# Kernel optimization log

Measured on AMD Instinct MI355X. Metric: run time of the kernel, lower is better.

## Reference

```python
import jax, jax.numpy as jnp
import numpy as np

B, T, E = 4, 2048, 2048
H, HKV, HD = 16, 8, 128
THETA = 10000.0
SCALE_BASE = 512.0


def _rotate_half(x):
    x1, x2 = jnp.split(x, 2, axis=-1)
    return jnp.concatenate([-x2, x1], axis=-1)


def _xpos_tables(seqlen):
    # cos/sin/scale tables for XPos rotary, all [seqlen, HD], fp32 compute dtype
    half_idx = jnp.arange(0, HD, 2, dtype=jnp.float32)
    inv_freq = 1.0 / (THETA ** (half_idx / HD))            # [HD/2]
    t = jnp.arange(seqlen, dtype=jnp.float32)
    freqs = jnp.outer(t, inv_freq)                          # [seqlen, HD/2]
    emb = jnp.concatenate([freqs, freqs], axis=-1)          # [seqlen, HD]
    cos, sin = jnp.cos(emb), jnp.sin(emb)
    # xpos decay: ((2i + 0.4d)/(1.4d)) ** ((t - L/2)/scale_base)
    scale_vec = (half_idx + 0.4 * HD) / (1.4 * HD)          # [HD/2]
    power = (t - seqlen // 2) / SCALE_BASE                  # [seqlen]
    scale = scale_vec[None, :] ** power[:, None]            # [seqlen, HD/2]
    scale = jnp.concatenate([scale, scale], axis=-1)        # [seqlen, HD]
    return cos, sin, scale


def setup_inputs() -> dict:
    key = jax.random.key(0)
    ks = jax.random.split(key, 5)
    std = 0.02
    return {
        "x": jax.random.normal(ks[0], (B, T, E), dtype=jnp.float32),
        "W_q": jax.random.normal(ks[1], (E, H * HD), dtype=jnp.float32) * std,
        "W_k": jax.random.normal(ks[2], (E, HKV * HD), dtype=jnp.float32) * std,
        "W_v": jax.random.normal(ks[3], (E, HKV * HD), dtype=jnp.float32) * std,
        "W_o": jax.random.normal(ks[4], (E, E), dtype=jnp.float32) * std,
    }


def reference(x, W_q, W_k, W_v, W_o):
    b, t, _ = x.shape
    q = (x @ W_q).reshape(b, t, H, HD)       # [B,T,H,HD]
    k = (x @ W_k).reshape(b, t, HKV, HD)     # [B,T,HKV,HD]
    v = (x @ W_v).reshape(b, t, HKV, HD)
    rep = H // HKV                            # GQA: repeat_interleave over head dim
    k = jnp.repeat(k, rep, axis=2)
    v = jnp.repeat(v, rep, axis=2)

    cos, sin, scale = _xpos_tables(t)         # past_len = 0 (no kv cache)
    cos = cos[None, :, None, :]
    sin = sin[None, :, None, :]
    scale = scale[None, :, None, :]
    q = q * scale
    q = q * cos + _rotate_half(q) * sin
    k = k / scale
    k = k * cos + _rotate_half(k) * sin

    inv_sqrt_d = 1.0 / jnp.sqrt(jnp.float32(HD))
    scores = jnp.einsum('bqhd,bkhd->bhqk', q, k) * inv_sqrt_d  # [B,H,T,T]
    causal = jnp.triu(jnp.ones((t, t), dtype=bool), k=1)
    scores = jnp.where(causal[None, None], -jnp.inf, scores)
    probs = jax.nn.softmax(scores, axis=-1)
    attn = jnp.einsum('bhqk,bkhd->bqhd', probs, v)             # [B,T,H,HD]
    out = attn.reshape(b, t, E) @ W_o
    return out
```

## Files before the change

### kernel.cpp

```cpp
#include <hip/hip_runtime.h>

typedef _Float16 f16;
typedef __attribute__((ext_vector_type(8))) _Float16 f16x8;
typedef __attribute__((ext_vector_type(4))) _Float16 f16x4;
typedef __attribute__((ext_vector_type(4))) float f32x4;
typedef __attribute__((ext_vector_type(16))) float f32x16;
typedef __attribute__((ext_vector_type(4))) unsigned u32x4;

#define T_SEQ 2048
#define NBATCH 4

__device__ __forceinline__ void gld_lds16(const f16* g, f16* l) {
    __builtin_amdgcn_global_load_lds((const __attribute__((address_space(1))) void*)g,
                                     (__attribute__((address_space(3))) void*)l, 16, 0, 0);
}

__device__ __forceinline__ unsigned pk2(float a, float b) {
    __attribute__((ext_vector_type(2))) __fp16 h = __builtin_amdgcn_cvt_pkrtz(a, b);
    return __builtin_bit_cast(unsigned, h);
}

__global__ __launch_bounds__(256) void k_prep(const float* __restrict__ x,
                                              const float* __restrict__ Wq,
                                              const float* __restrict__ Wk,
                                              const float* __restrict__ Wv,
                                              const float* __restrict__ Wo,
                                              f16* __restrict__ xh,
                                              f16* __restrict__ wqkvT,
                                              f16* __restrict__ woT,
                                              float* __restrict__ tab) {
    __shared__ float tile[32][33];
    int bidx = blockIdx.x;
    if (bidx < 16384) {
        int i = bidx * 256 + threadIdx.x;
        float4 v = ((const float4*)x)[i];
        f16x4 o = { (f16)v.x, (f16)v.y, (f16)v.z, (f16)v.w };
        ((f16x4*)xh)[i] = o;
        return;
    }
    bidx -= 16384;
    if (bidx >= 12288) {
        int i = (bidx - 12288) * 256 + threadIdx.x;
        int t = i >> 6, f = i & 63;
        float inv_freq = powf(10000.0f, -(2.0f * f) / 128.0f);
        float ang = (float)t * inv_freq;
        float sv = (2.0f * f + 51.2f) / 179.2f;
        float pw = ((float)t - 1024.0f) / 512.0f;
        tab[i] = cosf(ang);
        tab[131072 + i] = sinf(ang);
        tab[262144 + i] = powf(sv, pw);
        return;
    }
    const float* src; f16* dst; int N, bx, by;
    if (bidx < 4096)      { src = Wq; dst = wqkvT;                      N = 2048; bx = bidx & 63; by = bidx >> 6; }
    else if (bidx < 6144) { src = Wk; dst = wqkvT + (size_t)2048 * 2048; N = 1024; int t2 = bidx - 4096; bx = t2 & 31; by = t2 >> 5; }
    else if (bidx < 8192) { src = Wv; dst = wqkvT + (size_t)3072 * 2048; N = 1024; int t2 = bidx - 6144; bx = t2 & 31; by = t2 >> 5; }
    else                  { src = Wo; dst = woT;                        N = 2048; int t2 = bidx - 8192; bx = t2 & 63; by = t2 >> 6; }
    int n0 = bx * 32, k0 = by * 32;
    int tx = threadIdx.x & 31, ty = threadIdx.x >> 5;
#pragma unroll
    for (int j = 0; j < 32; j += 8)
        tile[ty + j][tx] = src[(size_t)(k0 + ty + j) * N + n0 + tx];
    __syncthreads();
#pragma unroll
    for (int j = 0; j < 32; j += 8)
        dst[(size_t)(n0 + ty + j) * 2048 + k0 + tx] = (f16)tile[tx][ty + j];
}

__global__ __launch_bounds__(256) void k_post(f16* __restrict__ qkv,
                                              f16* __restrict__ vtg,
                                              const float* __restrict__ tab) {
    int bidx = blockIdx.x;
    const int tid = threadIdx.x;
    if (bidx < 1024) {
        const int kt = bidx & 31, bk = bidx >> 5;
        const int b = bk >> 3, kvh = bk & 7;
        __shared__ f16 tile[64][132];
#pragma unroll
        for (int p = 0; p < 4; ++p) {
            int idx = p * 256 + tid;
            int r = idx >> 4, dc = (idx & 15) * 8;
            f16x8 v = *(const f16x8*)(qkv + (size_t)(b * T_SEQ + kt * 64 + r) * 4096 + 3072 + kvh * 128 + dc);
#pragma unroll
            for (int j = 0; j < 8; ++j) tile[r][dc + j] = v[j];
        }
        __syncthreads();
        f16* outb = vtg + (size_t)(bk * 32 + kt) * 8192;
#pragma unroll
        for (int p = 0; p < 4; ++p) {
            int c = p * 256 + tid;
            int kchunk = c >> 7, d = c & 127;
            f16x8 o;
#pragma unroll
            for (int j = 0; j < 8; ++j) o[j] = tile[kchunk * 8 + j][d];
            *(f16x8*)(outb + (size_t)c * 8) = o;
        }
        return;
    }
    int idx = (bidx - 1024) * 256 + tid;
    const int QTOT = NBATCH * T_SEQ * 16 * 64;
    int f, col0, bt;
    bool isQ = idx < QTOT;
    if (isQ) {
        f = idx & 63; int hh = (idx >> 6) & 15; bt = idx >> 10;
        col0 = hh * 128 + f;
    } else {
        int j = idx - QTOT;
        f = j & 63; int hh = (j >> 6) & 7; bt = j >> 9;
        col0 = 2048 + hh * 128 + f;
    }
    int t = bt & (T_SEQ - 1);
    float cs = tab[t * 64 + f], sn = tab[131072 + t * 64 + f], sc = tab[262144 + t * 64 + f];
    float mult = isQ ? sc * 0.08838834764831845f : 1.0f / sc;
    size_t p = (size_t)bt * 4096 + col0;
    float x1 = (float)qkv[p], x2 = (float)qkv[p + 64];
    qkv[p]      = (f16)((x1 * cs - x2 * sn) * mult);
    qkv[p + 64] = (f16)((x2 * cs + x1 * sn) * mult);
}

template <typename OutT>
__global__ __launch_bounds__(512, 1) void k_gemm256(const f16* __restrict__ A,
                                                    const f16* __restrict__ B,
                                                    OutT* __restrict__ C, int M, int N, int K) {
    extern __shared__ char smem[];
    f16* As = (f16*)smem;
    f16* Bs = (f16*)smem + 32768;
    const int tid = threadIdx.x, lane = tid & 63, w = tid >> 6;
    const int wr4 = w >> 1, wc2 = w & 1;
    const int cq = lane & 15, gq = lane >> 4;
    const int nbx = gridDim.x;
    const int bid0 = blockIdx.y * nbx + blockIdx.x;
    const int x = bid0 & 7, idx = bid0 >> 3;
    const int snb = (nbx == 16) ? 3 : 2;
    const int mt = (x >> 1) * 8 + (idx >> snb);
    const int nt = (x & 1) * (nbx >> 1) + (idx & ((nbx >> 1) - 1));
    const int m0 = mt * 256, n0 = nt * 256;
    const int KT = K >> 6;

    f32x4 acc[2][2][2][4] = {};
    f16x8 aL[2][2], aH[2][2], bL[4][2], bH[4][2];

    auto stageA = [&](int buf, int half, int t) {
#pragma unroll
        for (int r = 0; r < 2; ++r) {
            int cb = r * 512 + w * 64;
            int c = cb + lane;
            int row = c >> 3, cc = c & 7;
            gld_lds16(A + (size_t)(m0 + half * 128 + row) * K + t * 64 + ((cc ^ (row & 7)) * 8),
                      As + buf * 16384 + half * 8192 + cb * 8);
        }
    };
    auto stageB = [&](int buf, int half, int t) {
#pragma unroll
        for (int r = 0; r < 2; ++r) {
            int cb = r * 512 + w * 64;
            int c = cb + lane;
            int row = c >> 3, cc = c & 7;
            gld_lds16(B + (size_t)(n0 + half * 128 + row) * K + t * 64 + ((cc ^ (row & 7)) * 8),
                      Bs + buf * 16384 + half * 8192 + cb * 8);
        }
    };
    auto rdA = [&](int buf, int qr, f16x8 a[2][2]) {
#pragma unroll
        for (int mi = 0; mi < 2; ++mi)
#pragma unroll
            for (int ks = 0; ks < 2; ++ks) {
                int R = qr * 128 + wr4 * 32 + mi * 16 + cq;
                a[mi][ks] = *(const f16x8*)&As[buf * 16384 + R * 64 + (((ks * 4 + gq) ^ (cq & 7)) * 8)];
            }
    };
    auto rdB = [&](int buf, int qc, f16x8 b[4][2]) {
#pragma unroll
        for (int ni = 0; ni < 4; ++ni)
#pragma unroll
            for (int ks = 0; ks < 2; ++ks) {
                int R = qc * 128 + wc2 * 64 + ni * 16 + cq;
                b[ni][ks] = *(const f16x8*)&Bs[buf * 16384 + R * 64 + (((ks * 4 + gq) ^ (cq & 7)) * 8)];
            }
    };

    stageA(0, 0, 0); stageB(0, 0, 0); stageB(0, 1, 0); stageA(0, 1, 0);
    if (KT > 1) { stageA(1, 0, 1); stageB(1, 0, 1); stageB(1, 1, 1); }
    asm volatile("s_waitcnt vmcnt(6)");
    __builtin_amdgcn_s_barrier();

#pragma unroll 1
    for (int t = 0; t < KT; ++t) {
        const int buf = t & 1;
        rdA(buf, 0, aL); rdB(buf, 0, bL); rdB(buf, 1, bH); rdA(buf, 1, aH);
        __builtin_amdgcn_s_setprio(1);
#pragma unroll
        for (int mi = 0; mi < 2; ++mi)
#pragma unroll
            for (int ni = 0; ni < 4; ++ni)
#pragma unroll
                for (int ks = 0; ks < 2; ++ks)
                    acc[0][0][mi][ni] = __builtin_amdgcn_mfma_f32_16x16x32_f16(aL[mi][ks], bL[ni][ks], acc[0][0][mi][ni], 0, 0, 0);
        __builtin_amdgcn_s_setprio(0);
        if (t + 1 < KT) stageA(buf ^ 1, 1, t + 1);
        __builtin_amdgcn_s_setprio(1);
#pragma unroll
        for (int mi = 0; mi < 2; ++mi)
#pragma unroll
            for (int ni = 0; ni < 4; ++ni)
#pragma unroll
                for (int ks = 0; ks < 2; ++ks)
                    acc[0][1][mi][ni] = __builtin_amdgcn_mfma_f32_16x16x32_f16(aL[mi][ks], bH[ni][ks], acc[0][1][mi][ni], 0, 0, 0);
        __builtin_amdgcn_s_setprio(0);
        __builtin_amdgcn_s_barrier();
        if (t + 2 < KT) { stageA(buf, 0, t + 2); stageB(buf, 0, t + 2); stageB(buf, 1, t + 2); }
        __builtin_amdgcn_s_setprio(1);
#pragma unroll
        for (int mi = 0; mi < 2; ++mi)
#pragma unroll
            for (int ni = 0; ni < 4; ++ni)
#pragma unroll
                for (int ks = 0; ks < 2; ++ks)
                    acc[1][1][mi][ni] = __builtin_amdgcn_mfma_f32_16x16x32_f16(aH[mi][ks], bH[ni][ks], acc[1][1][mi][ni], 0, 0, 0);
#pragma unroll
        for (int mi = 0; mi < 2; ++mi)
#pragma unroll
            for (int ni = 0; ni < 4; ++ni)
#pragma unroll
                for (int ks = 0; ks < 2; ++ks)
                    acc[1][0][mi][ni] = __builtin_amdgcn_mfma_f32_16x16x32_f16(aH[mi][ks], bL[ni][ks], acc[1][0][mi][ni], 0, 0, 0);
        __builtin_amdgcn_s_setprio(0);
        if (t + 2 < KT)      asm volatile("s_waitcnt vmcnt(6)");
        else                 asm volatile("s_waitcnt vmcnt(0)");
        __builtin_amdgcn_s_barrier();
    }

#pragma unroll
    for (int qr = 0; qr < 2; ++qr)
#pragma unroll
        for (int qc = 0; qc < 2; ++qc)
#pragma unroll
            for (int mi = 0; mi < 2; ++mi)
#pragma unroll
                for (int ni = 0; ni < 4; ++ni)
#pragma unroll
                    for (int i = 0; i < 4; ++i) {
                        int row = m0 + qr * 128 + wr4 * 32 + mi * 16 + gq * 4 + i;
                        int col = n0 + qc * 128 + wc2 * 64 + ni * 16 + cq;
                        C[(size_t)row * N + col] = (OutT)acc[qr][qc][mi][ni][i];
                    }
}

__global__ __launch_bounds__(512) void k_attn(const f16* __restrict__ qkv,
                                              const f16* __restrict__ vtg,
                                              f16* __restrict__ ao) {
    extern __shared__ f16 asmem[];
    const int bid0 = blockIdx.x;
    const int bid = (bid0 & 7) * 32 + (bid0 >> 3);
    const int pr = bid & 7, kvh = (bid >> 3) & 7, b = bid >> 6;
    const int bk = b * 8 + kvh;
    const int tid = threadIdx.x, lane = tid & 63, w = tid >> 6;
    const int w4 = w & 3, hg = w >> 2;
    const int h = kvh * 2 + hg;
    const int l31 = lane & 31, hi = lane >> 5;

    const f16* kbase = qkv + (size_t)b * T_SEQ * 4096 + 2048 + kvh * 128;
    const f16* vbase = vtg + (size_t)bk * 32 * 8192;

    auto stage = [&](int buf, int kt) {
        f16* kb_ = asmem + buf * 16384;
        f16* vb_ = kb_ + 8192;
#pragma unroll
        for (int qq = 0; qq < 2; ++qq) {
            int c = w * 128 + qq * 64 + lane;
            int row = c >> 4;
            int ch = (c & 15) ^ (row & 15);
            gld_lds16(kbase + (size_t)(kt * 64 + row) * 4096 + ch * 8, kb_ + (w * 128 + qq * 64) * 8);
        }
#pragma unroll
        for (int qq = 0; qq < 2; ++qq) {
            int c = w * 128 + qq * 64 + lane;
            gld_lds16(vbase + ((size_t)kt * 1024 + c) * 8, vb_ + (w * 128 + qq * 64) * 8);
        }
    };

#pragma unroll 1
    for (int hf = 0; hf < 2; ++hf) {
        const int qt = hf ? pr : (15 - pr);
        const int q0 = qt * 128;
        const int nkt = 2 * qt + 2;
        const int qrow = q0 + w4 * 32 + l31;

        f16x8 qf[8];
#pragma unroll
        for (int ds = 0; ds < 8; ++ds)
            qf[ds] = *(const f16x8*)(qkv + (size_t)(b * T_SEQ + qrow) * 4096 + h * 128 + ds * 16 + hi * 8);

        f32x16 Ot[4] = {};
        float mrow = -1e30f, lrow = 0.0f;

        stage(0, 0);
        if (nkt > 1) stage(1, 1);

#pragma unroll 1
        for (int kt = 0; kt < nkt; ++kt) {
            const int kb = kt % 3;
            const f16* Kl = asmem + kb * 16384;
            const f16* Vl = Kl + 8192;
            if (kt + 1 < nkt) asm volatile("s_waitcnt vmcnt(4)");
            else              asm volatile("s_waitcnt vmcnt(0)");
            __builtin_amdgcn_s_barrier();

            if (!(kt == 2 * qt + 1 && w4 < 2)) {
                f32x16 St0 = {}, St1 = {};
                __builtin_amdgcn_s_setprio(1);
#pragma unroll
                for (int ds = 0; ds < 8; ++ds) {
                    int slot = (((2 * ds + hi) ^ (l31 & 15)) << 3);
                    f16x8 k0 = *(const f16x8*)&Kl[l31 * 128 + slot];
                    f16x8 k1 = *(const f16x8*)&Kl[(32 + l31) * 128 + slot];
                    St0 = __builtin_amdgcn_mfma_f32_32x32x16_f16(k0, qf[ds], St0, 0, 0, 0);
                    St1 = __builtin_amdgcn_mfma_f32_32x32x16_f16(k1, qf[ds], St1, 0, 0, 0);
                }
                __builtin_amdgcn_s_setprio(0);

                if (kt >= 2 * qt) {
                    int kbase2 = kt * 64;
#pragma unroll
                    for (int r = 0; r < 16; ++r) {
                        int krel = (r & 3) + 8 * (r >> 2) + 4 * hi;
                        if (kbase2 + krel > qrow) St0[r] = -1e30f;
                        if (kbase2 + 32 + krel > qrow) St1[r] = -1e30f;
                    }
                }

                float tm[16];
#pragma unroll
                for (int r = 0; r < 16; ++r) tm[r] = fmaxf(St0[r], St1[r]);
#pragma unroll
                for (int d = 8; d >= 1; d >>= 1)
#pragma unroll
                    for (int r = 0; r < 8; ++r)
                        if (r < d) tm[r] = fmaxf(tm[r], tm[r + d]);
                float tmax = tm[0];
                float mtile = fmaxf(tmax, __shfl_xor(tmax, 32, 64));

                if (!__all((mtile - mrow) <= 8.0f)) {
                    float mnew = fmaxf(mrow, mtile);
                    float fs = __expf(mrow - mnew);
                    mrow = mnew;
                    lrow *= fs;
#pragma unroll
                    for (int dblk = 0; dblk < 4; ++dblk)
#pragma unroll
                        for (int e = 0; e < 16; ++e) Ot[dblk][e] *= fs;
                }
#pragma unroll
                for (int r = 0; r < 16; ++r) {
                    St0[r] = __expf(St0[r] - mrow);
                    St1[r] = __expf(St1[r] - mrow);
                }
                float ts[16];
#pragma unroll
                for (int r = 0; r < 16; ++r) ts[r] = St0[r] + St1[r];
#pragma unroll
                for (int d = 8; d >= 1; d >>= 1)
#pragma unroll
                    for (int r = 0; r < 8; ++r)
                        if (r < d) ts[r] += ts[r + d];
                float tsum = ts[0];
                lrow += tsum + __shfl_xor(tsum, 32, 64);

#define PV_P(o, pos) ((o) < 4 ? St0[((o) & 3) * 4 + (pos)] : St1[((o) & 3) * 4 + (pos)])
#pragma unroll
                for (int s = 0; s < 4; ++s) {
                    unsigned x1 = pk2(PV_P(2 * s, 0), PV_P(2 * s, 1));
                    unsigned x2 = pk2(PV_P(2 * s, 2), PV_P(2 * s, 3));
                    unsigned y1 = pk2(PV_P(2 * s + 1, 0), PV_P(2 * s + 1, 1));
                    unsigned y2 = pk2(PV_P(2 * s + 1, 2), PV_P(2 * s + 1, 3));
                    unsigned sx1 = __shfl_xor(x1, 32, 64);
                    unsigned sx2 = __shfl_xor(x2, 32, 64);
                    unsigned sy1 = __shfl_xor(y1, 32, 64);
                    unsigned sy2 = __shfl_xor(y2, 32, 64);
                    u32x4 pw;
                    pw[0] = hi ? sy1 : x1;
                    pw[1] = hi ? sy2 : x2;
                    pw[2] = hi ? y1 : sx1;
                    pw[3] = hi ? y2 : sx2;
                    f16x8 pa = __builtin_bit_cast(f16x8, pw);
                    __builtin_amdgcn_s_setprio(1);
#pragma unroll
                    for (int dblk = 0; dblk < 4; ++dblk) {
                        f16x8 vb = *(const f16x8*)&Vl[(((2 * s + hi) << 7) + 32 * dblk + l31) << 3];
                        Ot[dblk] = __builtin_amdgcn_mfma_f32_32x32x16_f16(vb, pa, Ot[dblk], 0, 0, 0);
                    }
                    __builtin_amdgcn_s_setprio(0);
                }
#undef PV_P
            }
            __builtin_amdgcn_s_barrier();
            if (kt + 2 < nkt) stage((kt + 2) % 3, kt + 2);
        }

        {
            float inv = 1.0f / lrow;
            size_t rowb = (size_t)(b * T_SEQ + qrow) * 2048 + h * 128;
#pragma unroll
            for (int dblk = 0; dblk < 4; ++dblk)
#pragma unroll
                for (int rg = 0; rg < 4; ++rg) {
                    f16x4 o4 = { (f16)(Ot[dblk][rg * 4 + 0] * inv), (f16)(Ot[dblk][rg * 4 + 1] * inv),
                                 (f16)(Ot[dblk][rg * 4 + 2] * inv), (f16)(Ot[dblk][rg * 4 + 3] * inv) };
                    *(f16x4*)(ao + rowb + dblk * 32 + rg * 8 + hi * 4) = o4;
                }
        }
    }
}

extern "C" void kernel_launch(void* const* d_in, const int* in_sizes, int n_in,
                              void* d_out, int out_size, void* d_ws, size_t ws_size,
                              hipStream_t stream) {
    const float* x  = (const float*)d_in[0];
    const float* Wq = (const float*)d_in[1];
    const float* Wk = (const float*)d_in[2];
    const float* Wv = (const float*)d_in[3];
    const float* Wo = (const float*)d_in[4];
    float* out = (float*)d_out;

    f16* xh    = (f16*)d_ws;
    f16* wqkvT = xh + (size_t)16777216;
    f16* woT   = wqkvT + (size_t)8388608;
    f16* qkv   = woT + (size_t)4194304;
    float* tab = (float*)(qkv + (size_t)33554432);
    f16* ao  = xh;
    f16* vtg = wqkvT;

    hipFuncSetAttribute(reinterpret_cast<const void*>(&k_gemm256<f16>),
                        hipFuncAttributeMaxDynamicSharedMemorySize, 131072);
    hipFuncSetAttribute(reinterpret_cast<const void*>(&k_gemm256<float>),
                        hipFuncAttributeMaxDynamicSharedMemorySize, 131072);
    hipFuncSetAttribute(reinterpret_cast<const void*>(&k_attn),
                        hipFuncAttributeMaxDynamicSharedMemorySize, 98304);

    k_prep<<<29184, 256, 0, stream>>>(x, Wq, Wk, Wv, Wo, xh, wqkvT, woT, tab);
    k_gemm256<f16><<<dim3(16, 32), 512, 131072, stream>>>(xh, wqkvT, qkv, 8192, 4096, 2048);
    k_post<<<50176, 256, 0, stream>>>(qkv, vtg, tab);
    k_attn<<<256, 512, 98304, stream>>>(qkv, vtg, ao);
    k_gemm256<float><<<dim3(8, 32), 512, 131072, stream>>>(ao, woT, out, 8192, 2048, 2048);
}
```

Baseline: 366.3 us.

## Software-pipeline QK^T of next tile with softmax/PV of current tile

```diff
diff --git a/kernel.cpp b/kernel.cpp
--- a/kernel.cpp
+++ b/kernel.cpp
@@ -293,108 +293,131 @@
 
         f32x16 Ot[4] = {};
         float mrow = -1e30f, lrow = 0.0f;
-
-        stage(0, 0);
-        if (nkt > 1) stage(1, 1);
-
-#pragma unroll 1
-        for (int kt = 0; kt < nkt; ++kt) {
-            const int kb = kt % 3;
-            const f16* Kl = asmem + kb * 16384;
-            const f16* Vl = Kl + 8192;
-            if (kt + 1 < nkt) asm volatile("s_waitcnt vmcnt(4)");
-            else              asm volatile("s_waitcnt vmcnt(0)");
-            __builtin_amdgcn_s_barrier();
-
-            if (!(kt == 2 * qt + 1 && w4 < 2)) {
-                f32x16 St0 = {}, St1 = {};
+        f32x16 SA0 = {}, SA1 = {}, SB0 = {}, SB1 = {};
+
+        auto qkc = [&](int kt, f32x16& S0, f32x16& S1) {
+            const f16* Kl = asmem + (kt % 3) * 16384;
+            __builtin_amdgcn_s_setprio(1);
+#pragma unroll
+            for (int ds = 0; ds < 8; ++ds) {
+                int slot = (((2 * ds + hi) ^ (l31 & 15)) << 3);
+                f16x8 k0 = *(const f16x8*)&Kl[l31 * 128 + slot];
+                f16x8 k1 = *(const f16x8*)&Kl[(32 + l31) * 128 + slot];
+                S0 = __builtin_amdgcn_mfma_f32_32x32x16_f16(k0, qf[ds], S0, 0, 0, 0);
+                S1 = __builtin_amdgcn_mfma_f32_32x32x16_f16(k1, qf[ds], S1, 0, 0, 0);
+            }
+            __builtin_amdgcn_s_setprio(0);
+        };
+
+        auto proc = [&](int kt, f32x16& St0, f32x16& St1) {
+            if (kt == 2 * qt + 1 && w4 < 2) return;
+            const f16* Vl = asmem + (kt % 3) * 16384 + 8192;
+            if (kt >= 2 * qt) {
+                int kbase2 = kt * 64;
+#pragma unroll
+                for (int r = 0; r < 16; ++r) {
+                    int krel = (r & 3) + 8 * (r >> 2) + 4 * hi;
+                    if (kbase2 + krel > qrow) St0[r] = -1e30f;
+                    if (kbase2 + 32 + krel > qrow) St1[r] = -1e30f;
+                }
+            }
+            float tm[16];
+#pragma unroll
+            for (int r = 0; r < 16; ++r) tm[r] = fmaxf(St0[r], St1[r]);
+#pragma unroll
+            for (int d = 8; d >= 1; d >>= 1)
+#pragma unroll
+                for (int r = 0; r < 8; ++r)
+                    if (r < d) tm[r] = fmaxf(tm[r], tm[r + d]);
+            float tmax = tm[0];
+            float mtile = fmaxf(tmax, __shfl_xor(tmax, 32, 64));
+
+            if (!__all((mtile - mrow) <= 8.0f)) {
+                float mnew = fmaxf(mrow, mtile);
+                float fs = __expf(mrow - mnew);
+                mrow = mnew;
+                lrow *= fs;
+#pragma unroll
+                for (int dblk = 0; dblk < 4; ++dblk)
+#pragma unroll
+                    for (int e = 0; e < 16; ++e) Ot[dblk][e] *= fs;
+            }
+#pragma unroll
+            for (int r = 0; r < 16; ++r) {
+                St0[r] = __expf(St0[r] - mrow);
+                St1[r] = __expf(St1[r] - mrow);
+            }
+            float ts[16];
+#pragma unroll
+            for (int r = 0; r < 16; ++r) ts[r] = St0[r] + St1[r];
+#pragma unroll
+            for (int d = 8; d >= 1; d >>= 1)
+#pragma unroll
+                for (int r = 0; r < 8; ++r)
+                    if (r < d) ts[r] += ts[r + d];
+            float tsum = ts[0];
+            lrow += tsum + __shfl_xor(tsum, 32, 64);
+
+#define PV_P(o, pos) ((o) < 4 ? St0[((o) & 3) * 4 + (pos)] : St1[((o) & 3) * 4 + (pos)])
+#pragma unroll
+            for (int s = 0; s < 4; ++s) {
+                unsigned x1 = pk2(PV_P(2 * s, 0), PV_P(2 * s, 1));
+                unsigned x2 = pk2(PV_P(2 * s, 2), PV_P(2 * s, 3));
+                unsigned y1 = pk2(PV_P(2 * s + 1, 0), PV_P(2 * s + 1, 1));
+                unsigned y2 = pk2(PV_P(2 * s + 1, 2), PV_P(2 * s + 1, 3));
+                unsigned sx1 = __shfl_xor(x1, 32, 64);
+                unsigned sx2 = __shfl_xor(x2, 32, 64);
+                unsigned sy1 = __shfl_xor(y1, 32, 64);
+                unsigned sy2 = __shfl_xor(y2, 32, 64);
+                u32x4 pw;
+                pw[0] = hi ? sy1 : x1;
+                pw[1] = hi ? sy2 : x2;
+                pw[2] = hi ? y1 : sx1;
+                pw[3] = hi ? y2 : sx2;
+                f16x8 pa = __builtin_bit_cast(f16x8, pw);
                 __builtin_amdgcn_s_setprio(1);
 #pragma unroll
-                for (int ds = 0; ds < 8; ++ds) {
-                    int slot = (((2 * ds + hi) ^ (l31 & 15)) << 3);
-                    f16x8 k0 = *(const f16x8*)&Kl[l31 * 128 + slot];
-                    f16x8 k1 = *(const f16x8*)&Kl[(32 + l31) * 128 + slot];
-                    St0 = __builtin_amdgcn_mfma_f32_32x32x16_f16(k0, qf[ds], St0, 0, 0, 0);
-                    St1 = __builtin_amdgcn_mfma_f32_32x32x16_f16(k1, qf[ds], St1, 0, 0, 0);
+                for (int dblk = 0; dblk < 4; ++dblk) {
+                    f16x8 vb = *(const f16x8*)&Vl[(((2 * s + hi) << 7) + 32 * dblk + l31) << 3];
+                    Ot[dblk] = __builtin_amdgcn_mfma_f32_32x32x16_f16(vb, pa, Ot[dblk], 0, 0, 0);
                 }
                 __builtin_amdgcn_s_setprio(0);
-
-                if (kt >= 2 * qt) {
-                    int kbase2 = kt * 64;
-#pragma unroll
-                    for (int r = 0; r < 16; ++r) {
-                        int krel = (r & 3) + 8 * (r >> 2) + 4 * hi;
-                        if (kbase2 + krel > qrow) St0[r] = -1e30f;
-                        if (kbase2 + 32 + krel > qrow) St1[r] = -1e30f;
-                    }
-                }
-
-                float tm[16];
-#pragma unroll
-                for (int r = 0; r < 16; ++r) tm[r] = fmaxf(St0[r], St1[r]);
-#pragma unroll
-                for (int d = 8; d >= 1; d >>= 1)
-#pragma unroll
-                    for (int r = 0; r < 8; ++r)
-                        if (r < d) tm[r] = fmaxf(tm[r], tm[r + d]);
-                float tmax = tm[0];
-                float mtile = fmaxf(tmax, __shfl_xor(tmax, 32, 64));
-
-                if (!__all((mtile - mrow) <= 8.0f)) {
-                    float mnew = fmaxf(mrow, mtile);
-                    float fs = __expf(mrow - mnew);
-                    mrow = mnew;
-                    lrow *= fs;
-#pragma unroll
-                    for (int dblk = 0; dblk < 4; ++dblk)
-#pragma unroll
-                        for (int e = 0; e < 16; ++e) Ot[dblk][e] *= fs;
-                }
-#pragma unroll
-                for (int r = 0; r < 16; ++r) {
-                    St0[r] = __expf(St0[r] - mrow);
-                    St1[r] = __expf(St1[r] - mrow);
-                }
-                float ts[16];
-#pragma unroll
-                for (int r = 0; r < 16; ++r) ts[r] = St0[r] + St1[r];
-#pragma unroll
-                for (int d = 8; d >= 1; d >>= 1)
-#pragma unroll
-                    for (int r = 0; r < 8; ++r)
-                        if (r < d) ts[r] += ts[r + d];
-                float tsum = ts[0];
-                lrow += tsum + __shfl_xor(tsum, 32, 64);
-
-#define PV_P(o, pos) ((o) < 4 ? St0[((o) & 3) * 4 + (pos)] : St1[((o) & 3) * 4 + (pos)])
-#pragma unroll
-                for (int s = 0; s < 4; ++s) {
-                    unsigned x1 = pk2(PV_P(2 * s, 0), PV_P(2 * s, 1));
-                    unsigned x2 = pk2(PV_P(2 * s, 2), PV_P(2 * s, 3));
-                    unsigned y1 = pk2(PV_P(2 * s + 1, 0), PV_P(2 * s + 1, 1));
-                    unsigned y2 = pk2(PV_P(2 * s + 1, 2), PV_P(2 * s + 1, 3));
-                    unsigned sx1 = __shfl_xor(x1, 32, 64);
-                    unsigned sx2 = __shfl_xor(x2, 32, 64);
-                    unsigned sy1 = __shfl_xor(y1, 32, 64);
-                    unsigned sy2 = __shfl_xor(y2, 32, 64);
-                    u32x4 pw;
-                    pw[0] = hi ? sy1 : x1;
-                    pw[1] = hi ? sy2 : x2;
-                    pw[2] = hi ? y1 : sx1;
-                    pw[3] = hi ? y2 : sx2;
-                    f16x8 pa = __builtin_bit_cast(f16x8, pw);
-                    __builtin_amdgcn_s_setprio(1);
-#pragma unroll
-                    for (int dblk = 0; dblk < 4; ++dblk) {
-                        f16x8 vb = *(const f16x8*)&Vl[(((2 * s + hi) << 7) + 32 * dblk + l31) << 3];
-                        Ot[dblk] = __builtin_amdgcn_mfma_f32_32x32x16_f16(vb, pa, Ot[dblk], 0, 0, 0);
-                    }
-                    __builtin_amdgcn_s_setprio(0);
-                }
+            }
 #undef PV_P
+        };
+
+        stage(0, 0);
+        stage(1, 1);
+        asm volatile("s_waitcnt vmcnt(0)");
+        __builtin_amdgcn_s_barrier();
+        qkc(0, SA0, SA1);
+
+#pragma unroll 1
+        for (int kt = 0; kt < nkt; kt += 2) {
+            if (kt + 2 < nkt) {
+                stage((kt + 2) % 3, kt + 2);
+                asm volatile("s_waitcnt vmcnt(4)");
+            } else {
+                asm volatile("s_waitcnt vmcnt(0)");
             }
             __builtin_amdgcn_s_barrier();
-            if (kt + 2 < nkt) stage((kt + 2) % 3, kt + 2);
+            SB0 = f32x16{}; SB1 = f32x16{};
+            qkc(kt + 1, SB0, SB1);
+            proc(kt, SA0, SA1);
+            __builtin_amdgcn_s_barrier();
+            if (kt + 3 < nkt) {
+                stage((kt + 3) % 3, kt + 3);
+                asm volatile("s_waitcnt vmcnt(4)");
+            } else {
+                asm volatile("s_waitcnt vmcnt(0)");
+            }
+            __builtin_amdgcn_s_barrier();
+            if (kt + 2 < nkt) {
+                SA0 = f32x16{}; SA1 = f32x16{};
+                qkc(kt + 2, SA0, SA1);
+            }
+            proc(kt + 1, SB0, SB1);
+            __builtin_amdgcn_s_barrier();
         }
 
         {
```

Result: no change. 366.2 us (-0.0%).
